# Performance work log

Measured on AMD Instinct MI355X. Metric: run time of the kernel, lower is better.

## Reference

```python
import jax, jax.numpy as jnp
import numpy as np

NUM_NODES = 113      # nodes (ROIs) per graph, from __init__ default
NUM_GRAPHS = 4096    # graphs in the batch
IN_DIM, HID, EMB = 3, 128, 1024
GROUPS = 8
EPS = 1e-5


def _kaiming(key, fan_in, fan_out_dim, shape):
    # kaiming_normal_(mode='fan_out', nonlinearity='leaky_relu') with default a=sqrt(5)->gain irrelevant here;
    # torch uses gain = sqrt(2/(1+0.01^2)) for leaky_relu default slope; simple faithful-scale normal init.
    gain = jnp.sqrt(2.0 / (1.0 + 0.01 ** 2)).astype(jnp.float32)
    std = gain / jnp.sqrt(jnp.float32(fan_out_dim))
    return jax.random.normal(key, shape, dtype=jnp.float32) * std


def setup_inputs() -> dict:
    key = jax.random.key(0)
    ks = jax.random.split(key, 8)
    N = NUM_GRAPHS * NUM_NODES
    x = jax.random.normal(ks[0], (N, IN_DIM), dtype=jnp.float32)
    batch = jnp.repeat(jnp.arange(NUM_GRAPHS, dtype=jnp.int32), NUM_NODES)
    return {
        "x": x,
        "roi_scaler": jnp.ones((NUM_NODES, IN_DIM), dtype=jnp.float32),
        "W1": _kaiming(ks[1], IN_DIM, HID, (IN_DIM, HID)),
        "b1": jnp.zeros((HID,), jnp.float32),
        "gn_g": jnp.ones((HID,), jnp.float32),
        "gn_b": jnp.zeros((HID,), jnp.float32),
        "W2": _kaiming(ks[2], HID, HID, (HID, HID)),
        "b2": jnp.zeros((HID,), jnp.float32),
        "W3": _kaiming(ks[3], HID, 512, (HID, 512)),
        "b3": jnp.zeros((512,), jnp.float32),
        "bn_g": jnp.ones((512,), jnp.float32),
        "bn_b": jnp.zeros((512,), jnp.float32),
        "W4": _kaiming(ks[4], 512, EMB, (512, EMB)),
        "b4": jnp.zeros((EMB,), jnp.float32),
        "batch": batch,
    }


def _group_norm(h, gamma, beta):
    # torch GroupNorm on [N, C]: per-row, per-group normalization
    N, C = h.shape
    hg = h.reshape(N, GROUPS, C // GROUPS)
    mu = hg.mean(axis=-1, keepdims=True)
    var = hg.var(axis=-1, keepdims=True)
    hn = ((hg - mu) * jax.lax.rsqrt(var + EPS)).reshape(N, C)
    return hn * gamma + beta


def reference(x, roi_scaler, W1, b1, gn_g, gn_b, W2, b2, W3, b3, bn_g, bn_b, W4, b4, batch):
    # per-ROI learned scaling, tiled across graphs (node order is graph-major)
    h = x * jnp.tile(roi_scaler, (NUM_GRAPHS, 1))            # [N, 3]
    # node_net: Linear -> GroupNorm(8) -> LeakyReLU(0.2) -> Linear
    h = h @ W1 + b1                                          # [N, 128]
    h = _group_norm(h, gn_g, gn_b)
    h = jnp.where(h > 0, h, 0.2 * h)
    h = h @ W2 + b2                                          # [N, 128]
    # global_max_pool: segment max over graph id
    z = jax.ops.segment_max(h, batch, num_segments=NUM_GRAPHS)  # [G, 128]
    # projection: Linear -> BatchNorm1d (batch stats, no running stats) -> ReLU -> Linear
    p = z @ W3 + b3                                          # [G, 512]
    mu = p.mean(axis=0)
    var = p.var(axis=0)
    p = (p - mu) * jax.lax.rsqrt(var + EPS) * bn_g + bn_b
    p = jax.nn.relu(p)
    out = p @ W4 + b4                                        # [G, 1024]
    # F.normalize(p=2, dim=1)
    nrm = jnp.sqrt(jnp.sum(out * out, axis=1, keepdims=True))
    return out / jnp.maximum(nrm, 1e-12)
```

## Files before the change

### kernel.cpp

```cpp
#include <hip/hip_runtime.h>
#include <hip/hip_bf16.h>

typedef _Float16 f16_8 __attribute__((ext_vector_type(8)));
typedef _Float16 f16_4 __attribute__((ext_vector_type(4)));
typedef float f32x4 __attribute__((ext_vector_type(4)));

#define NNODES 113
#define NGRAPH 4096

#define Z_OFF    0u
#define PH_OFF   2097152u
#define PSUM_OFF 6291456u
#define PSQ_OFF  6815744u
#define GC_OFF   10485760u
#define SA_OFF   10489856u
#define SD_OFF   10491904u
#define W2P_OFF  10493952u
#define W4P_OFF  10559488u

__global__ __launch_bounds__(256) void k0_prep(
    const float* __restrict__ W2, const float* __restrict__ W4,
    const float* __restrict__ W1, const float* __restrict__ b1,
    _Float16* __restrict__ w2p, _Float16* __restrict__ w4p,
    float* __restrict__ gc) {
  int b = blockIdx.x, t = threadIdx.x;
  if (b < 256) {
    __shared__ _Float16 T[32 * 72];
    int kt = b >> 4, nc = b & 15;
    int row = t >> 3, c8 = (t & 7) * 8;
    const float* src = &W4[(kt * 32 + row) * 1024 + nc * 64 + c8];
    float4 a0 = *(const float4*)src;
    float4 a1 = *(const float4*)(src + 4);
    f16_8 v = {(_Float16)a0.x, (_Float16)a0.y, (_Float16)a0.z, (_Float16)a0.w,
               (_Float16)a1.x, (_Float16)a1.y, (_Float16)a1.z, (_Float16)a1.w};
    *(f16_8*)&T[row * 72 + c8] = v;
    __syncthreads();
    int ntl = t >> 6, L = t & 63;
    f16_8 w;
#pragma unroll
    for (int j = 0; j < 8; j++)
      w[j] = T[((L >> 4) * 8 + j) * 72 + ntl * 16 + (L & 15)];
    *(f16_8*)&w4p[((kt * 64 + nc * 4 + ntl) * 64 + L) * 8] = w;
  } else if (b < 264) {
    int q0 = (b - 256) * 256 + t;
    int L = q0 & 63, nt = (q0 >> 6) & 7, kt = q0 >> 9;
    f16_8 v;
#pragma unroll
    for (int j = 0; j < 8; j++)
      v[j] = (_Float16)W2[(kt * 32 + ((L >> 4) << 3) + j) * 128 + (nt << 4) + (L & 15)];
    *(f16_8*)&w2p[((kt * 8 + nt) * 64 + L) * 8] = v;
  } else {
    if (t < 128) {
      float a0 = W1[t], a1 = W1[128 + t], a2 = W1[256 + t], bb = b1[t];
      float p[14] = {a0, a1, a2, bb,
                     a0 * a0, 2.f * a0 * a1, 2.f * a0 * a2,
                     a1 * a1, 2.f * a1 * a2, a2 * a2,
                     2.f * bb * a0, 2.f * bb * a1, 2.f * bb * a2, bb * bb};
#pragma unroll
      for (int m = 1; m < 16; m <<= 1)
#pragma unroll
        for (int k = 0; k < 14; k++) p[k] += __shfl_xor(p[k], m, 64);
      if ((t & 15) == 0) {
        int gg = t >> 4;
#pragma unroll
        for (int k = 0; k < 4; k++) gc[gg * 16 + k] = p[k] * 0.0625f;
#pragma unroll
        for (int k = 4; k < 14; k++) gc[gg * 16 + k] = p[k];
      }
    }
  }
}

__global__ __launch_bounds__(256, 4) void k1_nodenet(
    const float* __restrict__ x, const float* __restrict__ roi,
    const float* __restrict__ W1, const float* __restrict__ b1,
    const float* __restrict__ gn_g, const float* __restrict__ gn_b,
    const _Float16* __restrict__ w2p, const float* __restrict__ b2,
    const float* __restrict__ gc, float* __restrict__ z) {
  __shared__ float4 xs4[NNODES];
  __shared__ _Float16 A[128 * 136];
  int t = threadIdx.x, g = blockIdx.x;
  int lane = t & 63, wv = t >> 6, quad = lane >> 4, l16 = lane & 15;

  int o = t & 15;
  int gq = o >> 1;
  float gcv[14];
#pragma unroll
  for (int j = 0; j < 14; j++) gcv[j] = gc[gq * 16 + j];

  float pw0[8], pw1[8], pw2[8], pb[8], pg[8], pbe[8];
#pragma unroll
  for (int j = 0; j < 8; j++) {
    int c = o * 8 + j;
    pw0[j] = W1[c]; pw1[j] = W1[128 + c]; pw2[j] = W1[256 + c];
    pb[j] = b1[c];  pg[j] = gn_g[c];      pbe[j] = gn_b[c];
  }

  f16_8 bh[4][2];
#pragma unroll
  for (int kt = 0; kt < 4; kt++)
#pragma unroll
    for (int ni = 0; ni < 2; ni++)
      bh[kt][ni] = *(const f16_8*)&w2p[((kt * 8 + wv * 2 + ni) * 64 + lane) * 8];

  for (int i = t; i < NNODES * 3; i += 256) {
    float v = x[g * (NNODES * 3) + i] * roi[i];
    ((float*)xs4)[(i / 3) * 4 + (i % 3)] = v;
  }
  __syncthreads();

  for (int it = t; it < 2048; it += 256) {
    int n = it >> 4;
    f16_8 hv;
    if (n < NNODES) {
      float4 xv = xs4[n];
      float mu = fmaf(xv.z, gcv[2], fmaf(xv.y, gcv[1], fmaf(xv.x, gcv[0], gcv[3])));
      float qf = fmaf(xv.z, gcv[12], fmaf(xv.y, gcv[11], fmaf(xv.x, gcv[10], gcv[13])));
      float u0 = fmaf(xv.z, gcv[6], fmaf(xv.y, gcv[5], xv.x * gcv[4]));
      qf = fmaf(xv.x, u0, qf);
      float u1 = fmaf(xv.z, gcv[8], xv.y * gcv[7]);
      qf = fmaf(xv.y, u1, qf);
      qf = fmaf(xv.z * xv.z, gcv[9], qf);
      float var = fmaxf(qf * 0.0625f - mu * mu, 0.0f);
      float ia = rsqrtf(var + 1e-5f);
      float ib = -mu * ia;
#pragma unroll
      for (int j = 0; j < 8; j++) {
        float h = fmaf(xv.z, pw2[j], fmaf(xv.y, pw1[j], fmaf(xv.x, pw0[j], pb[j])));
        float y = fmaf(fmaf(h, ia, ib), pg[j], pbe[j]);
        y = (y > 0.0f) ? y : 0.2f * y;
        hv[j] = (_Float16)y;
      }
    } else {
#pragma unroll
      for (int j = 0; j < 8; j++) hv[j] = (_Float16)0.f;
    }
    *(f16_8*)&A[n * 136 + o * 8] = hv;
  }
  __syncthreads();

  f32x4 acc[2][8];
#pragma unroll
  for (int a = 0; a < 2; a++)
#pragma unroll
    for (int m = 0; m < 8; m++) acc[a][m] = (f32x4){0.f, 0.f, 0.f, 0.f};

#pragma unroll
  for (int kt = 0; kt < 4; kt++) {
    f16_8 ah[8];
#pragma unroll
    for (int mt = 0; mt < 8; mt++)
      ah[mt] = *(const f16_8*)&A[(mt * 16 + l16) * 136 + kt * 32 + quad * 8];
#pragma unroll
    for (int ni = 0; ni < 2; ni++)
#pragma unroll
      for (int mt = 0; mt < 8; mt++)
        acc[ni][mt] = __builtin_amdgcn_mfma_f32_16x16x32_f16(ah[mt], bh[kt][ni], acc[ni][mt], 0, 0, 0);
  }

#pragma unroll
  for (int ni = 0; ni < 2; ni++) {
    int nt = wv * 2 + ni;
    float m = -3.4e38f;
#pragma unroll
    for (int mt = 0; mt < 8; mt++)
#pragma unroll
      for (int r = 0; r < 4; r++) {
        int row = mt * 16 + quad * 4 + r;
        if (row < NNODES) m = fmaxf(m, acc[ni][mt][r]);
      }
    m = fmaxf(m, __shfl_xor(m, 16, 64));
    m = fmaxf(m, __shfl_xor(m, 32, 64));
    if (quad == 0) {
      int col = nt * 16 + l16;
      z[g * 128 + col] = m + b2[col];
    }
  }
}

__global__ __launch_bounds__(256) void k2_proj(
    const float* __restrict__ z, const float* __restrict__ W3,
    const float* __restrict__ b3, _Float16* __restrict__ ph,
    float* __restrict__ psum, float* __restrict__ psq) {
  __shared__ float zs[16 * 128];
  __shared__ float reds[8 * 128];
  __shared__ float redq[8 * 128];
  int t = threadIdx.x;
  int rb = blockIdx.x >> 2, cbb = blockIdx.x & 3;
  int gr0 = rb * 16, cc0 = cbb * 128;
  for (int i = t; i < 2048; i += 256) zs[i] = z[gr0 * 128 + i];
  int cg = t & 31, rg = t >> 5;
  int cc = cc0 + cg * 4;
  float4 bb = *(const float4*)&b3[cc];
  float a0[4] = {0.f, 0.f, 0.f, 0.f}, a1[4] = {0.f, 0.f, 0.f, 0.f};
  __syncthreads();

#pragma unroll 8
  for (int k = 0; k < 128; k++) {
    float4 w = *(const float4*)&W3[k * 512 + cc];
    float z0 = zs[rg * 256 + k];
    float z1 = zs[rg * 256 + 128 + k];
    a0[0] = fmaf(z0, w.x, a0[0]); a0[1] = fmaf(z0, w.y, a0[1]);
    a0[2] = fmaf(z0, w.z, a0[2]); a0[3] = fmaf(z0, w.w, a0[3]);
    a1[0] = fmaf(z1, w.x, a1[0]); a1[1] = fmaf(z1, w.y, a1[1]);
    a1[2] = fmaf(z1, w.z, a1[2]); a1[3] = fmaf(z1, w.w, a1[3]);
  }
  int r0 = gr0 + rg * 2;
  f16_4 h0, h1;
  float s[4], q[4];
#pragma unroll
  for (int j = 0; j < 4; j++) {
    float v0 = a0[j] + ((float*)&bb)[j];
    float v1 = a1[j] + ((float*)&bb)[j];
    h0[j] = (_Float16)v0; h1[j] = (_Float16)v1;
    s[j] = v0 + v1;
    q[j] = fmaf(v0, v0, v1 * v1);
  }
  *(f16_4*)&ph[r0 * 512 + cc] = h0;
  *(f16_4*)&ph[(r0 + 1) * 512 + cc] = h1;
#pragma unroll
  for (int j = 0; j < 4; j++) {
    reds[rg * 128 + cg * 4 + j] = s[j];
    redq[rg * 128 + cg * 4 + j] = q[j];
  }
  __syncthreads();
  if (t < 128) {
    float ss = 0.f, qq = 0.f;
#pragma unroll
    for (int r = 0; r < 8; r++) { ss += reds[r * 128 + t]; qq += redq[r * 128 + t]; }
    psum[rb * 512 + cc0 + t] = ss;
    psq[rb * 512 + cc0 + t] = qq;
  }
}

__global__ __launch_bounds__(256) void k3_stats(
    const float* __restrict__ psum, const float* __restrict__ psq,
    const float* __restrict__ bn_g, const float* __restrict__ bn_b,
    float* __restrict__ sa, float* __restrict__ sd) {
  int t = threadIdx.x;
  int c = blockIdx.x * 8 + (t >> 5);
  int l = t & 31;
  float s = 0.f, q = 0.f;
#pragma unroll
  for (int i = 0; i < 8; i++) {
    int b = l + i * 32;
    s += psum[b * 512 + c];
    q += psq[b * 512 + c];
  }
#pragma unroll
  for (int m = 1; m < 32; m <<= 1) {
    s += __shfl_xor(s, m, 64);
    q += __shfl_xor(q, m, 64);
  }
  if (l == 0) {
    float mu = s * (1.0f / 4096.0f);
    float var = fmaxf(q * (1.0f / 4096.0f) - mu * mu, 0.0f);
    float sc = bn_g[c] * rsqrtf(var + 1e-5f);
    sa[c] = sc;
    sd[c] = bn_b[c] - mu * sc;
  }
}

__global__ __launch_bounds__(512) void k4_gemm(
    const _Float16* __restrict__ ph, const float* __restrict__ sa,
    const float* __restrict__ sd, const _Float16* __restrict__ w4p,
    const float* __restrict__ b4, float* __restrict__ out) {
  __shared__ _Float16 A[16 * 16 * 40];
  __shared__ float sas[512], sds[512];
  __shared__ float rowsq[8][16];
  __shared__ float rinv[16];
  int t = threadIdx.x;
  int rb = blockIdx.x;
  int lane = t & 63, w = t >> 6, quad = lane >> 4, l16 = lane & 15;

  sas[t] = sa[t];
  sds[t] = sd[t];

  const _Float16* p0 = &ph[(rb * 16 + w) * 512 + lane * 8];
  const _Float16* p1 = &ph[(rb * 16 + w + 8) * 512 + lane * 8];
  f16_8 pv0 = *(const f16_8*)p0;
  f16_8 pv1 = *(const f16_8*)p1;
  int nt0 = w * 8;
  f16_8 bf0[8], bf1[8];
#pragma unroll
  for (int ni = 0; ni < 8; ni++)
    bf0[ni] = *(const f16_8*)&w4p[((nt0 + ni) * 64 + lane) * 8];
  __syncthreads();

  {
    int kt_s = lane >> 2, c8 = lane & 3;
    f32x4 s0 = *(const f32x4*)&sas[lane * 8];
    f32x4 s1 = *(const f32x4*)&sas[lane * 8 + 4];
    f32x4 d0 = *(const f32x4*)&sds[lane * 8];
    f32x4 d1 = *(const f32x4*)&sds[lane * 8 + 4];
    f16_8 o0, o1;
#pragma unroll
    for (int j = 0; j < 4; j++) {
      float v = fmaf((float)pv0[j], s0[j], d0[j]);
      o0[j] = (_Float16)fmaxf(v, 0.f);
      v = fmaf((float)pv0[4 + j], s1[j], d1[j]);
      o0[4 + j] = (_Float16)fmaxf(v, 0.f);
      v = fmaf((float)pv1[j], s0[j], d0[j]);
      o1[j] = (_Float16)fmaxf(v, 0.f);
      v = fmaf((float)pv1[4 + j], s1[j], d1[j]);
      o1[4 + j] = (_Float16)fmaxf(v, 0.f);
    }
    *(f16_8*)&A[(kt_s * 16 + w) * 40 + c8 * 8] = o0;
    *(f16_8*)&A[(kt_s * 16 + w + 8) * 40 + c8 * 8] = o1;
  }
  __syncthreads();

  f32x4 acc[8];
#pragma unroll
  for (int ni = 0; ni < 8; ni++) acc[ni] = (f32x4){0.f, 0.f, 0.f, 0.f};

#pragma unroll
  for (int kt2 = 0; kt2 < 8; kt2++) {
    const int ktA = kt2 * 2, ktB = kt2 * 2 + 1;
#pragma unroll
    for (int ni = 0; ni < 8; ni++)
      bf1[ni] = *(const f16_8*)&w4p[(((ktA + 1) * 64 + nt0 + ni) * 64 + lane) * 8];
    f16_8 afA = *(const f16_8*)&A[(ktA * 16 + l16) * 40 + quad * 8];
#pragma unroll
    for (int ni = 0; ni < 8; ni++)
      acc[ni] = __builtin_amdgcn_mfma_f32_16x16x32_f16(afA, bf0[ni], acc[ni], 0, 0, 0);
    if (kt2 < 7) {
#pragma unroll
      for (int ni = 0; ni < 8; ni++)
        bf0[ni] = *(const f16_8*)&w4p[(((ktB + 1) * 64 + nt0 + ni) * 64 + lane) * 8];
    }
    f16_8 afB = *(const f16_8*)&A[(ktB * 16 + l16) * 40 + quad * 8];
#pragma unroll
    for (int ni = 0; ni < 8; ni++)
      acc[ni] = __builtin_amdgcn_mfma_f32_16x16x32_f16(afB, bf1[ni], acc[ni], 0, 0, 0);
  }

  float rsq[4] = {0.f, 0.f, 0.f, 0.f};
#pragma unroll
  for (int ni = 0; ni < 8; ni++) {
    float bv = b4[w * 128 + ni * 16 + l16];
#pragma unroll
    for (int r = 0; r < 4; r++) {
      float v = acc[ni][r] + bv;
      acc[ni][r] = v;
      rsq[r] = fmaf(v, v, rsq[r]);
    }
  }
#pragma unroll
  for (int m = 1; m < 16; m <<= 1)
#pragma unroll
    for (int r = 0; r < 4; r++) rsq[r] += __shfl_xor(rsq[r], m, 64);
  if (l16 == 0)
#pragma unroll
    for (int r = 0; r < 4; r++) rowsq[w][quad * 4 + r] = rsq[r];
  __syncthreads();
  if (t < 16) {
    float s = 0.f;
#pragma unroll
    for (int ww = 0; ww < 8; ww++) s += rowsq[ww][t];
    rinv[t] = 1.0f / fmaxf(sqrtf(s), 1e-12f);
  }
  __syncthreads();
#pragma unroll
  for (int r = 0; r < 4; r++) {
    float inv = rinv[quad * 4 + r];
    int obase = (rb * 16 + quad * 4 + r) * 1024 + w * 128 + l16;
#pragma unroll
    for (int ni = 0; ni < 8; ni++)
      out[obase + ni * 16] = acc[ni][r] * inv;
  }
}

extern "C" void kernel_launch(void* const* d_in, const int* in_sizes, int n_in,
                              void* d_out, int out_size, void* d_ws, size_t ws_size,
                              hipStream_t stream) {
  const float* x   = (const float*)d_in[0];
  const float* roi = (const float*)d_in[1];
  const float* W1  = (const float*)d_in[2];
  const float* b1  = (const float*)d_in[3];
  const float* gng = (const float*)d_in[4];
  const float* gnb = (const float*)d_in[5];
  const float* W2  = (const float*)d_in[6];
  const float* b2  = (const float*)d_in[7];
  const float* W3  = (const float*)d_in[8];
  const float* b3  = (const float*)d_in[9];
  const float* bng = (const float*)d_in[10];
  const float* bnb = (const float*)d_in[11];
  const float* W4  = (const float*)d_in[12];
  const float* b4  = (const float*)d_in[13];
  float* out = (float*)d_out;

  char* ws = (char*)d_ws;
  float*    z    = (float*)(ws + Z_OFF);
  _Float16* ph   = (_Float16*)(ws + PH_OFF);
  float*    psum = (float*)(ws + PSUM_OFF);
  float*    psq  = (float*)(ws + PSQ_OFF);
  float*    gc   = (float*)(ws + GC_OFF);
  float*    sa   = (float*)(ws + SA_OFF);
  float*    sd   = (float*)(ws + SD_OFF);
  _Float16* w2p  = (_Float16*)(ws + W2P_OFF);
  _Float16* w4p  = (_Float16*)(ws + W4P_OFF);

  k0_prep<<<265, 256, 0, stream>>>(W2, W4, W1, b1, w2p, w4p, gc);
  k1_nodenet<<<NGRAPH, 256, 0, stream>>>(x, roi, W1, b1, gng, gnb, w2p, b2, gc, z);
  k2_proj<<<1024, 256, 0, stream>>>(z, W3, b3, ph, psum, psq);
  k3_stats<<<64, 256, 0, stream>>>(psum, psq, bng, bnb, sa, sd);
  k4_gemm<<<256, 512, 0, stream>>>(ph, sa, sd, w4p, b4, out);
}
```

Measured before the change: 164.3 us.

## Move projection GEMM to fp16 MFMA with prepacked W3 and half-precision pooled features

Measured after the change: 154.3 us. -6.1%, faster.

```diff
diff --git a/kernel.cpp b/kernel.cpp
--- a/kernel.cpp
+++ b/kernel.cpp
@@ -8,7 +8,8 @@
 #define NNODES 113
 #define NGRAPH 4096
 
-#define Z_OFF    0u
+#define ZH_OFF   0u
+#define W3P_OFF  1048576u
 #define PH_OFF   2097152u
 #define PSUM_OFF 6291456u
 #define PSQ_OFF  6815744u
@@ -21,8 +22,9 @@
 __global__ __launch_bounds__(256) void k0_prep(
     const float* __restrict__ W2, const float* __restrict__ W4,
     const float* __restrict__ W1, const float* __restrict__ b1,
+    const float* __restrict__ W3,
     _Float16* __restrict__ w2p, _Float16* __restrict__ w4p,
-    float* __restrict__ gc) {
+    _Float16* __restrict__ w3p, float* __restrict__ gc) {
   int b = blockIdx.x, t = threadIdx.x;
   if (b < 256) {
     __shared__ _Float16 T[32 * 72];
@@ -49,7 +51,7 @@
     for (int j = 0; j < 8; j++)
       v[j] = (_Float16)W2[(kt * 32 + ((L >> 4) << 3) + j) * 128 + (nt << 4) + (L & 15)];
     *(f16_8*)&w2p[((kt * 8 + nt) * 64 + L) * 8] = v;
-  } else {
+  } else if (b == 264) {
     if (t < 128) {
       float a0 = W1[t], a1 = W1[128 + t], a2 = W1[256 + t], bb = b1[t];
       float p[14] = {a0, a1, a2, bb,
@@ -68,6 +70,14 @@
         for (int k = 4; k < 14; k++) gc[gg * 16 + k] = p[k];
       }
     }
+  } else {
+    int q1 = (b - 265) * 256 + t;
+    int L = q1 & 63, nt = (q1 >> 6) & 31, kt = q1 >> 11;
+    f16_8 v;
+#pragma unroll
+    for (int j = 0; j < 8; j++)
+      v[j] = (_Float16)W3[(kt * 32 + ((L >> 4) << 3) + j) * 512 + (nt << 4) + (L & 15)];
+    *(f16_8*)&w3p[((kt * 32 + nt) * 64 + L) * 8] = v;
   }
 }
 
@@ -76,7 +86,7 @@
     const float* __restrict__ W1, const float* __restrict__ b1,
     const float* __restrict__ gn_g, const float* __restrict__ gn_b,
     const _Float16* __restrict__ w2p, const float* __restrict__ b2,
-    const float* __restrict__ gc, float* __restrict__ z) {
+    const float* __restrict__ gc, _Float16* __restrict__ zh) {
   __shared__ float4 xs4[NNODES];
   __shared__ _Float16 A[128 * 136];
   int t = threadIdx.x, g = blockIdx.x;
@@ -173,63 +183,58 @@
     m = fmaxf(m, __shfl_xor(m, 32, 64));
     if (quad == 0) {
       int col = nt * 16 + l16;
-      z[g * 128 + col] = m + b2[col];
+      zh[g * 128 + col] = (_Float16)(m + b2[col]);
     }
   }
 }
 
 __global__ __launch_bounds__(256) void k2_proj(
-    const float* __restrict__ z, const float* __restrict__ W3,
+    const _Float16* __restrict__ zh, const _Float16* __restrict__ w3p,
     const float* __restrict__ b3, _Float16* __restrict__ ph,
     float* __restrict__ psum, float* __restrict__ psq) {
-  __shared__ float zs[16 * 128];
-  __shared__ float reds[8 * 128];
-  __shared__ float redq[8 * 128];
   int t = threadIdx.x;
-  int rb = blockIdx.x >> 2, cbb = blockIdx.x & 3;
-  int gr0 = rb * 16, cc0 = cbb * 128;
-  for (int i = t; i < 2048; i += 256) zs[i] = z[gr0 * 128 + i];
-  int cg = t & 31, rg = t >> 5;
-  int cc = cc0 + cg * 4;
-  float4 bb = *(const float4*)&b3[cc];
-  float a0[4] = {0.f, 0.f, 0.f, 0.f}, a1[4] = {0.f, 0.f, 0.f, 0.f};
-  __syncthreads();
-
-#pragma unroll 8
-  for (int k = 0; k < 128; k++) {
-    float4 w = *(const float4*)&W3[k * 512 + cc];
-    float z0 = zs[rg * 256 + k];
-    float z1 = zs[rg * 256 + 128 + k];
-    a0[0] = fmaf(z0, w.x, a0[0]); a0[1] = fmaf(z0, w.y, a0[1]);
-    a0[2] = fmaf(z0, w.z, a0[2]); a0[3] = fmaf(z0, w.w, a0[3]);
-    a1[0] = fmaf(z1, w.x, a1[0]); a1[1] = fmaf(z1, w.y, a1[1]);
-    a1[2] = fmaf(z1, w.z, a1[2]); a1[3] = fmaf(z1, w.w, a1[3]);
-  }
-  int r0 = gr0 + rg * 2;
-  f16_4 h0, h1;
-  float s[4], q[4];
-#pragma unroll
-  for (int j = 0; j < 4; j++) {
-    float v0 = a0[j] + ((float*)&bb)[j];
-    float v1 = a1[j] + ((float*)&bb)[j];
-    h0[j] = (_Float16)v0; h1[j] = (_Float16)v1;
-    s[j] = v0 + v1;
-    q[j] = fmaf(v0, v0, v1 * v1);
-  }
-  *(f16_4*)&ph[r0 * 512 + cc] = h0;
-  *(f16_4*)&ph[(r0 + 1) * 512 + cc] = h1;
-#pragma unroll
-  for (int j = 0; j < 4; j++) {
-    reds[rg * 128 + cg * 4 + j] = s[j];
-    redq[rg * 128 + cg * 4 + j] = q[j];
-  }
-  __syncthreads();
-  if (t < 128) {
-    float ss = 0.f, qq = 0.f;
-#pragma unroll
-    for (int r = 0; r < 8; r++) { ss += reds[r * 128 + t]; qq += redq[r * 128 + t]; }
-    psum[rb * 512 + cc0 + t] = ss;
-    psq[rb * 512 + cc0 + t] = qq;
+  int rb = blockIdx.x >> 1, cb = blockIdx.x & 1;
+  int lane = t & 63, w = t >> 6, quad = lane >> 4, l16 = lane & 15;
+
+  f16_8 bf[4][4];
+#pragma unroll
+  for (int kt = 0; kt < 4; kt++)
+#pragma unroll
+    for (int ni = 0; ni < 4; ni++)
+      bf[kt][ni] = *(const f16_8*)&w3p[((kt * 32 + cb * 16 + w * 4 + ni) * 64 + lane) * 8];
+
+  const _Float16* za = &zh[(rb * 16 + l16) * 128 + quad * 8];
+  f32x4 acc[4];
+#pragma unroll
+  for (int ni = 0; ni < 4; ni++) acc[ni] = (f32x4){0.f, 0.f, 0.f, 0.f};
+#pragma unroll
+  for (int kt = 0; kt < 4; kt++) {
+    f16_8 af = *(const f16_8*)&za[kt * 32];
+#pragma unroll
+    for (int ni = 0; ni < 4; ni++)
+      acc[ni] = __builtin_amdgcn_mfma_f32_16x16x32_f16(af, bf[kt][ni], acc[ni], 0, 0, 0);
+  }
+
+#pragma unroll
+  for (int ni = 0; ni < 4; ni++) {
+    int col = cb * 256 + w * 64 + ni * 16 + l16;
+    float bv = b3[col];
+    float sx = 0.f, qx = 0.f;
+#pragma unroll
+    for (int r = 0; r < 4; r++) {
+      float v = acc[ni][r] + bv;
+      ph[(rb * 16 + quad * 4 + r) * 512 + col] = (_Float16)v;
+      sx += v;
+      qx = fmaf(v, v, qx);
+    }
+    sx += __shfl_xor(sx, 16, 64);
+    sx += __shfl_xor(sx, 32, 64);
+    qx += __shfl_xor(qx, 16, 64);
+    qx += __shfl_xor(qx, 32, 64);
+    if (quad == 0) {
+      psum[rb * 512 + col] = sx;
+      psq[rb * 512 + col] = qx;
+    }
   }
 }
 
@@ -391,7 +396,8 @@
   float* out = (float*)d_out;
 
   char* ws = (char*)d_ws;
-  float*    z    = (float*)(ws + Z_OFF);
+  _Float16* zh   = (_Float16*)(ws + ZH_OFF);
+  _Float16* w3p  = (_Float16*)(ws + W3P_OFF);
   _Float16* ph   = (_Float16*)(ws + PH_OFF);
   float*    psum = (float*)(ws + PSUM_OFF);
   float*    psq  = (float*)(ws + PSQ_OFF);
@@ -401,9 +407,9 @@
   _Float16* w2p  = (_Float16*)(ws + W2P_OFF);
   _Float16* w4p  = (_Float16*)(ws + W4P_OFF);
 
-  k0_prep<<<265, 256, 0, stream>>>(W2, W4, W1, b1, w2p, w4p, gc);
-  k1_nodenet<<<NGRAPH, 256, 0, stream>>>(x, roi, W1, b1, gng, gnb, w2p, b2, gc, z);
-  k2_proj<<<1024, 256, 0, stream>>>(z, W3, b3, ph, psum, psq);
+  k0_prep<<<297, 256, 0, stream>>>(W2, W4, W1, b1, W3, w2p, w4p, w3p, gc);
+  k1_nodenet<<<NGRAPH, 256, 0, stream>>>(x, roi, W1, b1, gng, gnb, w2p, b2, gc, zh);
+  k2_proj<<<512, 256, 0, stream>>>(zh, w3p, b3, ph, psum, psq);
   k3_stats<<<64, 256, 0, stream>>>(psum, psq, bng, bnb, sa, sd);
   k4_gemm<<<256, 512, 0, stream>>>(ph, sa, sd, w4p, b4, out);
 }
```
